# Kernel optimization log

Hardware: AMD Instinct MI355X
Metric: run time of the kernel (lower is better)

## Reference

```python
import jax, jax.numpy as jnp
import numpy as np

NEG_BIG = -1e12
ALPHA = 0.2  # LeakyReLU negative slope

def setup_inputs() -> dict:
    key = jax.random.key(0)
    k1, k2, k3, k4, k5 = jax.random.split(key, 5)
    N, F_in, F_out = 8192, 256, 128
    inp = jax.random.normal(k1, (N, F_in), dtype=jnp.float32)
    adj = jax.random.randint(k2, (N, N), 0, 2, dtype=jnp.int32)
    W = jax.random.normal(k3, (F_in, F_out), dtype=jnp.float32) * 0.05
    W_2 = jax.random.normal(k4, (F_in, F_out), dtype=jnp.float32) * 0.05
    W_3 = jax.random.normal(k5, (F_in, F_out), dtype=jnp.float32) * 0.05
    return {"inp": inp, "adj": adj, "W": W, "W_2": W_2, "W_3": W_3}

def reference(inp, adj, W, W_2, W_3):
    # h = inp @ W, h_2 = inp @ W_2  -> scores e = LeakyReLU(h @ h_2^T)  [N, N]
    h = inp @ W
    h_2 = inp @ W_2
    e = jax.nn.leaky_relu(h @ h_2.T, negative_slope=ALPHA)
    # adjacency mask, row softmax (dropout disabled: eval mode)
    attention = jax.nn.softmax(jnp.where(adj > 0, e, NEG_BIG), axis=1)
    h_3 = inp @ W_3
    h_prime = attention @ h_3
    return jax.nn.elu(h_prime)  # concat=True path
```

## Files before the change

kernel.cpp:

```cpp
#include <hip/hip_runtime.h>
#include <hip/hip_fp16.h>

#define N    8192
#define FIN  256
#define FOUT 128
#define BN   64

typedef _Float16 half8 __attribute__((ext_vector_type(8)));
typedef _Float16 half4v __attribute__((ext_vector_type(4)));
typedef float floatx4 __attribute__((ext_vector_type(4)));

__global__ __launch_bounds__(256)
void wprep_kernel(const float* __restrict__ W0,
                  const float* __restrict__ W1,
                  const float* __restrict__ W2,
                  _Float16* __restrict__ Wf)
{
    int idx  = blockIdx.x * 256 + threadIdx.x;
    int lane = idx & 63;
    int frag = idx >> 6;
    int w    = frag >> 6;
    int f    = frag & 63;
    int nt   = f >> 3, kc = f & 7;
    int quad = lane >> 4, lo16 = lane & 15;
    const float* Wp = w == 0 ? W0 : (w == 1 ? W1 : W2);
    half8 v;
#pragma unroll
    for (int jj = 0; jj < 8; jj++)
        v[jj] = (_Float16)Wp[(size_t)(kc * 32 + quad * 8 + jj) * FOUT + nt * 16 + lo16];
    *(half8*)&Wf[(size_t)idx * 8] = v;
}

__global__ __launch_bounds__(256, 2)
void gemm3_kernel(const float* __restrict__ inp,
                  const _Float16* __restrict__ Wf,
                  _Float16* __restrict__ H,
                  _Float16* __restrict__ H2,
                  _Float16* __restrict__ H3T)
{
    const int which = blockIdx.z;
    const int c0    = blockIdx.y * 64;
    const _Float16* Wfw = Wf + (size_t)which * 64 * 64 * 8;
    const int r0 = blockIdx.x * 64;
    const int tid  = threadIdx.x;
    const int wave = tid >> 6;
    const int lane = tid & 63;
    const int lo16 = lane & 15;
    const int quad = lane >> 4;
    const int r = r0 + wave * 16 + lo16;

    half8 a[8];
#pragma unroll
    for (int kc = 0; kc < 8; kc++) {
        const float* p = &inp[(size_t)r * FIN + kc * 32 + quad * 8];
        float4 v0 = *(const float4*)p;
        float4 v1 = *(const float4*)(p + 4);
        a[kc][0] = (_Float16)v0.x; a[kc][1] = (_Float16)v0.y;
        a[kc][2] = (_Float16)v0.z; a[kc][3] = (_Float16)v0.w;
        a[kc][4] = (_Float16)v1.x; a[kc][5] = (_Float16)v1.y;
        a[kc][6] = (_Float16)v1.z; a[kc][7] = (_Float16)v1.w;
    }

    floatx4 acc[4];
#pragma unroll
    for (int i = 0; i < 4; i++) acc[i] = (floatx4){0.f, 0.f, 0.f, 0.f};

#pragma unroll
    for (int kc = 0; kc < 8; kc++)
#pragma unroll
        for (int nt = 0; nt < 4; nt++) {
            int ntg = (c0 >> 4) + nt;
            half8 b = *(const half8*)&Wfw[(((size_t)ntg * 8 + kc) * 64 + lane) * 8];
            acc[nt] = __builtin_amdgcn_mfma_f32_16x16x32_f16(a[kc], b, acc[nt], 0, 0, 0);
        }

    const int arow = wave * 16 + quad * 4;
    if (which < 2) {
        _Float16* outp = which == 0 ? H : H2;
#pragma unroll
        for (int nt = 0; nt < 4; nt++)
#pragma unroll
            for (int rr = 0; rr < 4; rr++)
                outp[(size_t)(r0 + arow + rr) * FOUT + c0 + nt * 16 + lo16] = (_Float16)acc[nt][rr];
    } else {
#pragma unroll
        for (int nt = 0; nt < 4; nt++) {
            half4v v;
#pragma unroll
            for (int rr = 0; rr < 4; rr++) v[rr] = (_Float16)acc[nt][rr];
            *(half4v*)&H3T[(size_t)(c0 + nt * 16 + lo16) * N + r0 + arow] = v;
        }
    }
}

__global__ __launch_bounds__(256)
void repackKV_kernel(const _Float16* __restrict__ H2,
                     const _Float16* __restrict__ H3T,
                     _Float16* __restrict__ Kf,
                     _Float16* __restrict__ Vf)
{
    if (blockIdx.x < 512) {
        int idx  = blockIdx.x * 256 + threadIdx.x;
        int lane = idx & 63;
        int frag = idx >> 6;
        int jb = frag >> 4, f = frag & 15;
        int c = f >> 3, ntj = (f >> 2) & 1, kc = f & 3;
        int quad = lane >> 4, lo16 = lane & 15;
        int srcrow = jb * 64 + c * 32 + (lo16 >> 2) * 8 + ntj * 4 + (lo16 & 3);
        half8 v = *(const half8*)&H2[(size_t)srcrow * FOUT + kc * 32 + quad * 8];
        *(half8*)&Kf[(size_t)idx * 8] = v;
    } else {
        int idx  = (blockIdx.x - 512) * 256 + threadIdx.x;
        int lane = idx & 63;
        int frag = idx >> 6;
        int jb = frag >> 4, f = frag & 15, nt = f >> 1, kc = f & 1;
        int quad = lane >> 4, lo16 = lane & 15;
        half8 v = *(const half8*)&H3T[(size_t)(nt * 16 + lo16) * N + jb * 64 + kc * 32 + quad * 8];
        *(half8*)&Vf[(size_t)idx * 8] = v;
    }
}

template<int JS>
__global__ __launch_bounds__(256, 2)
void attn_kernel(const _Float16* __restrict__ Hq,
                 const _Float16* __restrict__ Kf,
                 const _Float16* __restrict__ Vf,
                 const int* __restrict__ adj,
                 float* __restrict__ OpartT,
                 float* __restrict__ mpart,
                 float* __restrict__ lpart)
{
    __shared__ _Float16 KV[2][16384];

    const int tid  = threadIdx.x;
    const int wave = tid >> 6;
    const int lane = tid & 63;
    const int lo16 = lane & 15;
    const int quad = lane >> 4;
    const int bid  = blockIdx.x;
    const int js   = bid & (JS - 1);
    const int ib   = bid / JS;
    const int iw   = ib * 128 + wave * 32;
    const int jbeg = js * (N / JS);
    const int NIT  = (N / JS) / BN;

    half8 q[2][4];
#pragma unroll
    for (int isub = 0; isub < 2; isub++)
#pragma unroll
        for (int kc = 0; kc < 4; kc++)
            q[isub][kc] = *(const half8*)&Hq[(size_t)(iw + isub * 16 + lo16) * FOUT + kc * 32 + quad * 8];

    floatx4 O[8][2];
#pragma unroll
    for (int nt = 0; nt < 8; nt++)
#pragma unroll
        for (int s = 0; s < 2; s++) O[nt][s] = (floatx4){0.f, 0.f, 0.f, 0.f};
    float m_s[2] = {-1e12f, -1e12f}, l_s[2] = {0.f, 0.f};

    int av[32];
    {
        const int* ap = adj + (size_t)iw * N + jbeg + lane;
#pragma unroll
        for (int x = 0; x < 32; x++) av[x] = ap[(size_t)x * N];
    }

    {
        const int jb0 = jbeg >> 6;
        const _Float16* gk = Kf + (size_t)jb0 * 8192;
        const _Float16* gv = Vf + (size_t)jb0 * 8192;
#pragma unroll
        for (int r = 0; r < 4; r++) {
            int off = (r * 256 + tid) * 8;
            *(half8*)&KV[0][off]        = *(const half8*)&gk[off];
            *(half8*)&KV[0][8192 + off] = *(const half8*)&gv[off];
        }
        __syncthreads();
    }

    int cur = 0;
    for (int it = 0; it < NIT; it++) {
        const int j0 = jbeg + it * BN;

        unsigned long long mw0 = 0, mw1 = 0;
#pragma unroll
        for (int x = 0; x < 16; x++) {
            unsigned long long b0 = __ballot(av[x] != 0);
            unsigned long long b1 = __ballot(av[x + 16] != 0);
            bool sel = (lo16 == x);
            mw0 = sel ? b0 : mw0;
            mw1 = sel ? b1 : mw1;
        }
        unsigned long long mw[2] = {mw0, mw1};

        half8 st[8];
        if (it + 1 < NIT) {
            const int jbn = (j0 + BN) >> 6;
            const _Float16* gk = Kf + (size_t)jbn * 8192;
            const _Float16* gv = Vf + (size_t)jbn * 8192;
#pragma unroll
            for (int r = 0; r < 4; r++) {
                int off = (r * 256 + tid) * 8;
                st[r]     = *(const half8*)&gk[off];
                st[r + 4] = *(const half8*)&gv[off];
            }
        }

        if (it + 1 < NIT) {
            const int* ap = adj + (size_t)iw * N + (j0 + BN) + lane;
#pragma unroll
            for (int x = 0; x < 32; x++) av[x] = ap[(size_t)x * N];
        }

        const _Float16* kb = &KV[cur][0];
        const _Float16* vb = &KV[cur][8192];

        floatx4 S[2][2][2];
#pragma unroll
        for (int c = 0; c < 2; c++)
#pragma unroll
            for (int ntj = 0; ntj < 2; ntj++) {
                S[c][ntj][0] = (floatx4){0.f, 0.f, 0.f, 0.f};
                S[c][ntj][1] = (floatx4){0.f, 0.f, 0.f, 0.f};
#pragma unroll
                for (int kc = 0; kc < 4; kc++) {
                    half8 kf = *(const half8*)&kb[(((c * 2 + ntj) * 4 + kc) * 64 + lane) * 8];
                    S[c][ntj][0] = __builtin_amdgcn_mfma_f32_16x16x32_f16(kf, q[0][kc], S[c][ntj][0], 0, 0, 0);
                    S[c][ntj][1] = __builtin_amdgcn_mfma_f32_16x16x32_f16(kf, q[1][kc], S[c][ntj][1], 0, 0, 0);
                }
            }

        float alpha[2];
#pragma unroll
        for (int s = 0; s < 2; s++) {
            float mx = -1e12f;
#pragma unroll
            for (int c = 0; c < 2; c++)
#pragma unroll
                for (int ntj = 0; ntj < 2; ntj++)
#pragma unroll
                    for (int r = 0; r < 4; r++) {
                        float e = S[c][ntj][s][r];
                        e = e > 0.f ? e : 0.2f * e;
                        mx = fmaxf(mx, e);
                    }
            mx = fmaxf(mx, __shfl_xor(mx, 16));
            mx = fmaxf(mx, __shfl_xor(mx, 32));
            float mn = fmaxf(m_s[s], mx);
            alpha[s] = __expf(m_s[s] - mn);
            m_s[s] = mn;
        }

        half8 pb[2][2];
        float sum[2] = {0.f, 0.f};
#pragma unroll
        for (int s = 0; s < 2; s++) {
            unsigned long long mq = mw[s] >> (quad * 8);
#pragma unroll
            for (int c = 0; c < 2; c++)
#pragma unroll
                for (int ntj = 0; ntj < 2; ntj++)
#pragma unroll
                    for (int r = 0; r < 4; r++) {
                        float e = S[c][ntj][s][r];
                        e = e > 0.f ? e : 0.2f * e;
                        bool bit = (mq >> (c * 32 + ntj * 4 + r)) & 1ull;
                        float p = bit ? __expf(e - m_s[s]) : 0.f;
                        sum[s] += p;
                        pb[s][c][ntj * 4 + r] = (_Float16)p;
                    }
            sum[s] += __shfl_xor(sum[s], 16);
            sum[s] += __shfl_xor(sum[s], 32);
            l_s[s] = l_s[s] * alpha[s] + sum[s];
#pragma unroll
            for (int nt = 0; nt < 8; nt++)
#pragma unroll
                for (int r = 0; r < 4; r++)
                    O[nt][s][r] *= alpha[s];
        }

#pragma unroll
        for (int c = 0; c < 2; c++)
#pragma unroll
            for (int nt = 0; nt < 8; nt++) {
                half8 vf = *(const half8*)&vb[((nt * 2 + c) * 64 + lane) * 8];
                O[nt][0] = __builtin_amdgcn_mfma_f32_16x16x32_f16(vf, pb[0][c], O[nt][0], 0, 0, 0);
                O[nt][1] = __builtin_amdgcn_mfma_f32_16x16x32_f16(vf, pb[1][c], O[nt][1], 0, 0, 0);
            }

        if (it + 1 < NIT) {
            const int nxt = cur ^ 1;
#pragma unroll
            for (int r = 0; r < 4; r++) {
                int off = (r * 256 + tid) * 8;
                *(half8*)&KV[nxt][off]        = st[r];
                *(half8*)&KV[nxt][8192 + off] = st[r + 4];
            }
        }
        __syncthreads();
        cur ^= 1;
    }

#pragma unroll
    for (int nt = 0; nt < 8; nt++)
#pragma unroll
        for (int s = 0; s < 2; s++)
#pragma unroll
            for (int r = 0; r < 4; r++) {
                int f = nt * 16 + quad * 4 + r;
                int i = iw + s * 16 + lo16;
                OpartT[((size_t)js * FOUT + f) * N + i] = O[nt][s][r];
            }
    if (quad == 0) {
#pragma unroll
        for (int s = 0; s < 2; s++) {
            mpart[js * N + iw + s * 16 + lo16] = m_s[s];
            lpart[js * N + iw + s * 16 + lo16] = l_s[s];
        }
    }
}

template<int JS>
__global__ __launch_bounds__(256)
void combine_kernel(const float* __restrict__ OpartT,
                    const float* __restrict__ mpart,
                    const float* __restrict__ lpart,
                    float* __restrict__ out)
{
    int idx = blockIdx.x * 256 + threadIdx.x;
    int f  = idx >> 11;
    int i4 = (idx & 2047) << 2;

    float4 M = {-3e38f, -3e38f, -3e38f, -3e38f};
    float4 m[JS];
#pragma unroll
    for (int s = 0; s < JS; s++) {
        m[s] = *(const float4*)&mpart[s * N + i4];
        M.x = fmaxf(M.x, m[s].x); M.y = fmaxf(M.y, m[s].y);
        M.z = fmaxf(M.z, m[s].z); M.w = fmaxf(M.w, m[s].w);
    }
    float4 L = {0.f, 0.f, 0.f, 0.f};
    float4 w[JS];
#pragma unroll
    for (int s = 0; s < JS; s++) {
        float4 l = *(const float4*)&lpart[s * N + i4];
        w[s].x = __expf(m[s].x - M.x); w[s].y = __expf(m[s].y - M.y);
        w[s].z = __expf(m[s].z - M.z); w[s].w = __expf(m[s].w - M.w);
        L.x += l.x * w[s].x; L.y += l.y * w[s].y;
        L.z += l.z * w[s].z; L.w += l.w * w[s].w;
    }
    float4 o = {0.f, 0.f, 0.f, 0.f};
#pragma unroll
    for (int s = 0; s < JS; s++) {
        float4 v = *(const float4*)&OpartT[((size_t)s * FOUT + f) * N + i4];
        o.x += w[s].x * v.x; o.y += w[s].y * v.y;
        o.z += w[s].z * v.z; o.w += w[s].w * v.w;
    }
    float r0 = o.x / L.x, r1 = o.y / L.y, r2 = o.z / L.z, r3 = o.w / L.w;
    out[(size_t)(i4 + 0) * FOUT + f] = r0 > 0.f ? r0 : __expf(r0) - 1.f;
    out[(size_t)(i4 + 1) * FOUT + f] = r1 > 0.f ? r1 : __expf(r1) - 1.f;
    out[(size_t)(i4 + 2) * FOUT + f] = r2 > 0.f ? r2 : __expf(r2) - 1.f;
    out[(size_t)(i4 + 3) * FOUT + f] = r3 > 0.f ? r3 : __expf(r3) - 1.f;
}

extern "C" void kernel_launch(void* const* d_in, const int* in_sizes, int n_in,
                              void* d_out, int out_size, void* d_ws, size_t ws_size,
                              hipStream_t stream) {
    const float* inp = (const float*)d_in[0];
    const int*   adj = (const int*)d_in[1];
    const float* W0  = (const float*)d_in[2];
    const float* W1  = (const float*)d_in[3];
    const float* W2  = (const float*)d_in[4];
    float* out = (float*)d_out;

    constexpr int JS = 8;
    char* ws = (char*)d_ws;
    _Float16* H    = (_Float16*)(ws);
    _Float16* H2   = (_Float16*)(ws + (2u << 20));
    _Float16* H3T  = (_Float16*)(ws + (4u << 20));
    _Float16* Wf   = (_Float16*)(ws + (6u << 20));
    _Float16* Kf   = (_Float16*)(ws + (7u << 20));
    _Float16* Vf   = (_Float16*)(ws + (9u << 20));
    float* OpartT  = (float*)(ws + (11u << 20));
    float* mpart   = (float*)(ws + (43u << 20));
    float* lpart   = (float*)(ws + (43u << 20) + (size_t)JS * N * sizeof(float));

    wprep_kernel<<<48, 256, 0, stream>>>(W0, W1, W2, Wf);
    gemm3_kernel<<<dim3(N / 64, 2, 3), 256, 0, stream>>>(inp, Wf, H, H2, H3T);
    repackKV_kernel<<<1024, 256, 0, stream>>>(H2, H3T, Kf, Vf);
    attn_kernel<JS><<<(N / 128) * JS, 256, 0, stream>>>(H, Kf, Vf, adj, OpartT, mpart, lpart);
    combine_kernel<JS><<<(FOUT * (N / 4)) / 256, 256, 0, stream>>>(OpartT, mpart, lpart, out);
}
```

Before: 428.6 us.

## Prepack adjacency bitmask, drop LDS K/V staging, use exp2 with lazy rescale

Adds a kernel that converts the int32 adjacency matrix into 64-bit row bitmasks, so the attention kernel loads two words per iteration instead of 32 strided int loads plus ballots. The attention kernel now reads K/V fragments directly from global/L2 instead of double-buffering through LDS with barriers. H is prescaled by log2(e) so softmax uses hardware exp2. The running max is only rescaled when it grows beyond a threshold, trading a bounded fp16 range for fewer rescales of O.

```diff
diff --git a/kernel.cpp b/kernel.cpp
--- a/kernel.cpp
+++ b/kernel.cpp
@@ -9,6 +9,8 @@
 typedef _Float16 half8 __attribute__((ext_vector_type(8)));
 typedef _Float16 half4v __attribute__((ext_vector_type(4)));
 typedef float floatx4 __attribute__((ext_vector_type(4)));
+
+__device__ __forceinline__ float exp2_fast(float x) { return __builtin_amdgcn_exp2f(x); }
 
 __global__ __launch_bounds__(256)
 void wprep_kernel(const float* __restrict__ W0,
@@ -77,11 +79,13 @@
     const int arow = wave * 16 + quad * 4;
     if (which < 2) {
         _Float16* outp = which == 0 ? H : H2;
+        const float scale = which == 0 ? 1.44269504f : 1.0f;
 #pragma unroll
         for (int nt = 0; nt < 4; nt++)
 #pragma unroll
             for (int rr = 0; rr < 4; rr++)
-                outp[(size_t)(r0 + arow + rr) * FOUT + c0 + nt * 16 + lo16] = (_Float16)acc[nt][rr];
+                outp[(size_t)(r0 + arow + rr) * FOUT + c0 + nt * 16 + lo16] =
+                    (_Float16)(acc[nt][rr] * scale);
     } else {
 #pragma unroll
         for (int nt = 0; nt < 4; nt++) {
@@ -120,18 +124,36 @@
     }
 }
 
+__global__ __launch_bounds__(256)
+void adjpack_kernel(const int* __restrict__ adj,
+                    unsigned long long* __restrict__ adjb)
+{
+    const int gw   = (blockIdx.x * 256 + threadIdx.x) >> 6;
+    const int lane = threadIdx.x & 63;
+    const int NW   = 2048 * 4;
+    for (int t = gw; t < N * 32; t += NW) {
+        int row = t >> 5, c4 = t & 31;
+        const int* p = adj + (size_t)row * N + c4 * 256 + lane;
+        int a0 = p[0], a1 = p[64], a2 = p[128], a3 = p[192];
+        unsigned long long b0 = __ballot(a0 != 0);
+        unsigned long long b1 = __ballot(a1 != 0);
+        unsigned long long b2 = __ballot(a2 != 0);
+        unsigned long long b3 = __ballot(a3 != 0);
+        unsigned long long v = lane == 0 ? b0 : (lane == 1 ? b1 : (lane == 2 ? b2 : b3));
+        if (lane < 4) adjb[(size_t)row * (N / 64) + c4 * 4 + lane] = v;
+    }
+}
+
 template<int JS>
 __global__ __launch_bounds__(256, 2)
 void attn_kernel(const _Float16* __restrict__ Hq,
                  const _Float16* __restrict__ Kf,
                  const _Float16* __restrict__ Vf,
-                 const int* __restrict__ adj,
+                 const unsigned long long* __restrict__ adjb,
                  float* __restrict__ OpartT,
                  float* __restrict__ mpart,
                  float* __restrict__ lpart)
 {
-    __shared__ _Float16 KV[2][16384];
-
     const int tid  = threadIdx.x;
     const int wave = tid >> 6;
     const int lane = tid & 63;
@@ -158,62 +180,13 @@
         for (int s = 0; s < 2; s++) O[nt][s] = (floatx4){0.f, 0.f, 0.f, 0.f};
     float m_s[2] = {-1e12f, -1e12f}, l_s[2] = {0.f, 0.f};
 
-    int av[32];
-    {
-        const int* ap = adj + (size_t)iw * N + jbeg + lane;
-#pragma unroll
-        for (int x = 0; x < 32; x++) av[x] = ap[(size_t)x * N];
-    }
-
-    {
-        const int jb0 = jbeg >> 6;
-        const _Float16* gk = Kf + (size_t)jb0 * 8192;
-        const _Float16* gv = Vf + (size_t)jb0 * 8192;
-#pragma unroll
-        for (int r = 0; r < 4; r++) {
-            int off = (r * 256 + tid) * 8;
-            *(half8*)&KV[0][off]        = *(const half8*)&gk[off];
-            *(half8*)&KV[0][8192 + off] = *(const half8*)&gv[off];
-        }
-        __syncthreads();
-    }
-
-    int cur = 0;
+    const unsigned long long* ar0 = adjb + (size_t)(iw + lo16) * (N / 64) + (jbeg >> 6);
+    const unsigned long long* ar1 = ar0 + (size_t)16 * (N / 64);
+
     for (int it = 0; it < NIT; it++) {
-        const int j0 = jbeg + it * BN;
-
-        unsigned long long mw0 = 0, mw1 = 0;
-#pragma unroll
-        for (int x = 0; x < 16; x++) {
-            unsigned long long b0 = __ballot(av[x] != 0);
-            unsigned long long b1 = __ballot(av[x + 16] != 0);
-            bool sel = (lo16 == x);
-            mw0 = sel ? b0 : mw0;
-            mw1 = sel ? b1 : mw1;
-        }
-        unsigned long long mw[2] = {mw0, mw1};
-
-        half8 st[8];
-        if (it + 1 < NIT) {
-            const int jbn = (j0 + BN) >> 6;
-            const _Float16* gk = Kf + (size_t)jbn * 8192;
-            const _Float16* gv = Vf + (size_t)jbn * 8192;
-#pragma unroll
-            for (int r = 0; r < 4; r++) {
-                int off = (r * 256 + tid) * 8;
-                st[r]     = *(const half8*)&gk[off];
-                st[r + 4] = *(const half8*)&gv[off];
-            }
-        }
-
-        if (it + 1 < NIT) {
-            const int* ap = adj + (size_t)iw * N + (j0 + BN) + lane;
-#pragma unroll
-            for (int x = 0; x < 32; x++) av[x] = ap[(size_t)x * N];
-        }
-
-        const _Float16* kb = &KV[cur][0];
-        const _Float16* vb = &KV[cur][8192];
+        const _Float16* kb = Kf + (size_t)((jbeg >> 6) + it) * 8192;
+        const _Float16* vb = Vf + (size_t)((jbeg >> 6) + it) * 8192;
+        unsigned long long mw[2] = { ar0[it], ar1[it] };
 
         floatx4 S[2][2][2];
 #pragma unroll
@@ -230,7 +203,7 @@
                 }
             }
 
-        float alpha[2];
+        half8 pb[2][2];
 #pragma unroll
         for (int s = 0; s < 2; s++) {
             float mx = -1e12f;
@@ -241,42 +214,42 @@
 #pragma unroll
                     for (int r = 0; r < 4; r++) {
                         float e = S[c][ntj][s][r];
-                        e = e > 0.f ? e : 0.2f * e;
+                        e = fmaxf(e, 0.2f * e);
+                        S[c][ntj][s][r] = e;
                         mx = fmaxf(mx, e);
                     }
             mx = fmaxf(mx, __shfl_xor(mx, 16));
             mx = fmaxf(mx, __shfl_xor(mx, 32));
-            float mn = fmaxf(m_s[s], mx);
-            alpha[s] = __expf(m_s[s] - mn);
-            m_s[s] = mn;
-        }
-
-        half8 pb[2][2];
-        float sum[2] = {0.f, 0.f};
-#pragma unroll
-        for (int s = 0; s < 2; s++) {
+            if (__any(mx > m_s[s] + 5.75f)) {
+                float mn = fmaxf(m_s[s], mx);
+                float al = exp2_fast(m_s[s] - mn);
+                m_s[s] = mn;
+                l_s[s] *= al;
+#pragma unroll
+                for (int nt = 0; nt < 8; nt++)
+#pragma unroll
+                    for (int r = 0; r < 4; r++)
+                        O[nt][s][r] *= al;
+            }
+
             unsigned long long mq = mw[s] >> (quad * 8);
+            unsigned mh[2] = { (unsigned)mq, (unsigned)(mq >> 32) };
+            float sum = 0.f;
 #pragma unroll
             for (int c = 0; c < 2; c++)
 #pragma unroll
                 for (int ntj = 0; ntj < 2; ntj++)
 #pragma unroll
                     for (int r = 0; r < 4; r++) {
-                        float e = S[c][ntj][s][r];
-                        e = e > 0.f ? e : 0.2f * e;
-                        bool bit = (mq >> (c * 32 + ntj * 4 + r)) & 1ull;
-                        float p = bit ? __expf(e - m_s[s]) : 0.f;
-                        sum[s] += p;
+                        float e = S[c][ntj][s][r] - m_s[s];
+                        bool bit = (mh[c] >> (ntj * 4 + r)) & 1u;
+                        float p = bit ? exp2_fast(e) : 0.f;
+                        sum += p;
                         pb[s][c][ntj * 4 + r] = (_Float16)p;
                     }
-            sum[s] += __shfl_xor(sum[s], 16);
-            sum[s] += __shfl_xor(sum[s], 32);
-            l_s[s] = l_s[s] * alpha[s] + sum[s];
-#pragma unroll
-            for (int nt = 0; nt < 8; nt++)
-#pragma unroll
-                for (int r = 0; r < 4; r++)
-                    O[nt][s][r] *= alpha[s];
+            sum += __shfl_xor(sum, 16);
+            sum += __shfl_xor(sum, 32);
+            l_s[s] += sum;
         }
 
 #pragma unroll
@@ -287,18 +260,6 @@
                 O[nt][0] = __builtin_amdgcn_mfma_f32_16x16x32_f16(vf, pb[0][c], O[nt][0], 0, 0, 0);
                 O[nt][1] = __builtin_amdgcn_mfma_f32_16x16x32_f16(vf, pb[1][c], O[nt][1], 0, 0, 0);
             }
-
-        if (it + 1 < NIT) {
-            const int nxt = cur ^ 1;
-#pragma unroll
-            for (int r = 0; r < 4; r++) {
-                int off = (r * 256 + tid) * 8;
-                *(half8*)&KV[nxt][off]        = st[r];
-                *(half8*)&KV[nxt][8192 + off] = st[r + 4];
-            }
-        }
-        __syncthreads();
-        cur ^= 1;
     }
 
 #pragma unroll
@@ -344,8 +305,8 @@
 #pragma unroll
     for (int s = 0; s < JS; s++) {
         float4 l = *(const float4*)&lpart[s * N + i4];
-        w[s].x = __expf(m[s].x - M.x); w[s].y = __expf(m[s].y - M.y);
-        w[s].z = __expf(m[s].z - M.z); w[s].w = __expf(m[s].w - M.w);
+        w[s].x = exp2_fast(m[s].x - M.x); w[s].y = exp2_fast(m[s].y - M.y);
+        w[s].z = exp2_fast(m[s].z - M.z); w[s].w = exp2_fast(m[s].w - M.w);
         L.x += l.x * w[s].x; L.y += l.y * w[s].y;
         L.z += l.z * w[s].z; L.w += l.w * w[s].w;
     }
@@ -384,10 +345,12 @@
     float* OpartT  = (float*)(ws + (11u << 20));
     float* mpart   = (float*)(ws + (43u << 20));
     float* lpart   = (float*)(ws + (43u << 20) + (size_t)JS * N * sizeof(float));
+    unsigned long long* adjb = (unsigned long long*)(ws + (44u << 20));
 
     wprep_kernel<<<48, 256, 0, stream>>>(W0, W1, W2, Wf);
     gemm3_kernel<<<dim3(N / 64, 2, 3), 256, 0, stream>>>(inp, Wf, H, H2, H3T);
     repackKV_kernel<<<1024, 256, 0, stream>>>(H2, H3T, Kf, Vf);
-    attn_kernel<JS><<<(N / 128) * JS, 256, 0, stream>>>(H, Kf, Vf, adj, OpartT, mpart, lpart);
+    adjpack_kernel<<<2048, 256, 0, stream>>>(adj, adjb);
+    attn_kernel<JS><<<(N / 128) * JS, 256, 0, stream>>>(H, Kf, Vf, adjb, OpartT, mpart, lpart);
     combine_kernel<JS><<<(FOUT * (N / 4)) / 256, 256, 0, stream>>>(OpartT, mpart, lpart, out);
 }
```

Result: slower. 596.4 us (+39.2%).
